# Kernel optimization log

Hardware: AMD Instinct MI355X
Metric: run time of the kernel (lower is better)

The kernel has to match this reference:

```python
import jax, jax.numpy as jnp
import numpy as np

B, C_IN, NF, H, W, L = 8, 64, 64, 96, 96, 13
NEG_SLOPE = 0.2


def conv2d(x, w, b, pad):
    # x: [B,C,H,W], w: [O,I,kh,kw]
    y = jax.lax.conv_general_dilated(
        x, w, window_strides=(1, 1), padding=[(pad, pad), (pad, pad)],
        dimension_numbers=("NCHW", "OIHW", "NCHW"))
    return y + b[None, :, None, None]


def leaky(x):
    return jax.nn.leaky_relu(x, NEG_SLOPE)


def bilinear_sample(img, px, py):
    # img: [B,C,H,W]; px,py: [B,H,W] pixel coords; zero padding outside.
    Bs, C, Hs, Ws = img.shape
    x0 = jnp.floor(px)
    y0 = jnp.floor(py)
    wx = px - x0
    wy = py - y0
    x0i = x0.astype(jnp.int32)
    y0i = y0.astype(jnp.int32)
    imgf = img.reshape(Bs, C, Hs * Ws)

    def gather(xi, yi):
        valid = ((xi >= 0) & (xi < Ws) & (yi >= 0) & (yi < Hs)).astype(img.dtype)
        xc = jnp.clip(xi, 0, Ws - 1)
        yc = jnp.clip(yi, 0, Hs - 1)
        idx = (yc * Ws + xc).reshape(Bs, 1, Hs * Ws)
        v = jnp.take_along_axis(imgf, idx, axis=2).reshape(Bs, C, Hs, Ws)
        return v * valid[:, None, :, :]

    return (gather(x0i, y0i) * ((1 - wx) * (1 - wy))[:, None]
            + gather(x0i + 1, y0i) * (wx * (1 - wy))[:, None]
            + gather(x0i, y0i + 1) * ((1 - wx) * wy)[:, None]
            + gather(x0i + 1, y0i + 1) * (wx * wy)[:, None])


def warp(img, flow):
    # img: [B,C,H,W]; flow: [B,2,H,W] (dx=flow[:,0], dy=flow[:,1])
    Bs, C, Hs, Ws = img.shape
    xx = jnp.arange(Ws, dtype=img.dtype)[None, None, :]  # [1,1,W]
    yy = jnp.arange(Hs, dtype=img.dtype)[None, :, None]  # [1,H,1]
    vx = xx + flow[:, 0]  # [B,H,W]
    vy = yy + flow[:, 1]
    # torch grid_sample(align_corners=False) with normalization 2*v/(dim-1)-1:
    # sample pixel = v*dim/(dim-1) - 0.5
    px = vx * (Ws / (Ws - 1)) - 0.5
    py = vy * (Hs / (Hs - 1)) - 0.5
    return bilinear_sample(img, px, py)


def setup_inputs() -> dict:
    key = jax.random.key(0)
    ks = jax.random.split(key, 13)
    s = 0.05
    return {
        "x": jax.random.normal(ks[0], (B, C_IN, H, W), jnp.float32),
        "m": jax.random.normal(ks[1], (B, NF, H, W), jnp.float32),
        "prev_h": jax.random.normal(ks[2], (B, NF, H, W), jnp.float32),
        "w_i2h": jax.random.normal(ks[3], (3 * NF, C_IN, 3, 3), jnp.float32) * s,
        "b_i2h": jnp.zeros((3 * NF,), jnp.float32),
        "w_i2f": jax.random.normal(ks[4], (32, C_IN, 5, 5), jnp.float32) * s,
        "b_i2f": jnp.zeros((32,), jnp.float32),
        "w_h2f": jax.random.normal(ks[5], (32, NF, 5, 5), jnp.float32) * s,
        "b_h2f": jnp.zeros((32,), jnp.float32),
        "w_fl": jax.random.normal(ks[6], (2 * L, 32, 5, 5), jnp.float32) * s,
        "b_fl": jnp.zeros((2 * L,), jnp.float32),
        "w_ret": jax.random.normal(ks[7], (3 * NF, NF * L, 1, 1), jnp.float32) * s,
        "b_ret": jnp.zeros((3 * NF,), jnp.float32),
    }


def reference(x, m, prev_h, w_i2h, b_i2h, w_i2f, b_i2f, w_h2f, b_h2f, w_fl, b_fl, w_ret, b_ret):
    # input-to-hidden gates
    i2h = conv2d(x, w_i2h, b_i2h, pad=1)              # [B,3NF,H,W]
    i0, i1, i2 = jnp.split(i2h, 3, axis=1)
    # flow generator
    f = leaky(conv2d(x, w_i2f, b_i2f, pad=2) + conv2d(prev_h, w_h2f, b_h2f, pad=2))
    flows = conv2d(f, w_fl, b_fl, pad=2)              # [B,2L,H,W]
    flows = flows.reshape(B, L, 2, H, W)
    # warp prev_h by -flow for each link (vectorized over L)
    warped = jax.vmap(lambda fl: warp(prev_h, -fl), in_axes=1, out_axes=1)(flows)
    warped = warped.reshape(B, L * NF, H, W)
    h2h = conv2d(warped, w_ret, b_ret, pad=0)         # [B,3NF,H,W]
    h0, h1, h2 = jnp.split(h2h, 3, axis=1)
    reset_gate = jax.nn.sigmoid(i0 + h0)
    update_gate = jax.nn.sigmoid(i1 + h1)
    new_mem = leaky(i2 + reset_gate * h2)
    next_h = update_gate * prev_h + (1.0 - update_gate) * new_mem
    return (next_h, m, next_h)
```

## Files before the change

kernel.cpp:

```cpp
#include <hip/hip_runtime.h>
#include <hip/hip_bf16.h>
#include <hip/hip_fp16.h>

typedef unsigned short u16;
typedef unsigned int u32;
typedef __attribute__((ext_vector_type(8))) _Float16 f16x8;
typedef __attribute__((ext_vector_type(4))) float f32x4;

#define NEG 0.2f

__device__ __forceinline__ float bf2f(u16 u) {
    return __uint_as_float(((u32)u) << 16);
}
__device__ __forceinline__ u16 f2b(float f) {
    u32 u = __float_as_uint(f);
    u32 r = (u + 0x7FFF + ((u >> 16) & 1)) >> 16;
    return (u16)r;
}
__device__ __forceinline__ u16 f2h(float f) {
    return __half_as_ushort(__float2half(f));
}
__device__ __forceinline__ float h2f(u16 u) {
    return __half2float(__ushort_as_half(u));
}
__device__ __forceinline__ float sigm(float x) {
    return 1.0f / (1.0f + __expf(-x));
}
__device__ __forceinline__ float ldin(const void* p, int idx, int flag) {
    if (flag) return ((const float*)p)[idx];
    return bf2f(((const u16*)p)[idx]);
}
__device__ __forceinline__ u16 ldin_h(const void* p, int idx, int flag) {
    if (flag) return f2h(((const float*)p)[idx]);
    return f2h(bf2f(((const u16*)p)[idx]));
}


#define WS_NEED 60371008u

__global__ void kdetect(const u16* __restrict__ x, u32* __restrict__ flag)
{
    __shared__ u32 mx[256];
    int t = threadIdx.x;
    u32 m = 0;
    for (int i = t; i < 8192; i += 256) {
        u32 e = ((u32)x[i] >> 7) & 0xFF;
        m = m > e ? m : e;
    }
    mx[t] = m;
    __syncthreads();
    for (int s = 128; s > 0; s >>= 1) {
        if (t < s) mx[t] = mx[t] > mx[t + s] ? mx[t] : mx[t + s];
        __syncthreads();
    }
    if (t == 0) flag[0] = (mx[0] > 0xC0) ? 1u : 0u;
}

__global__ void kprep(const void* __restrict__ w_i2h, const void* __restrict__ w_i2f,
                      const void* __restrict__ w_h2f, const void* __restrict__ w_fl,
                      const void* __restrict__ w_ret,
                      const void* __restrict__ b_i2h, const void* __restrict__ b_i2f,
                      const void* __restrict__ b_h2f, const void* __restrict__ b_fl,
                      const void* __restrict__ b_ret,
                      u16* __restrict__ wiA, u16* __restrict__ wfA,
                      u16* __restrict__ wlA, u16* __restrict__ wretA,
                      float* __restrict__ biases, const u32* __restrict__ flag)
{
    int flg = (int)flag[0];
    int i = blockIdx.x * 256 + threadIdx.x;
    if (i < 110592) {
        int j = i & 7; int lane = (i >> 3) & 63; int rest = i >> 9;
        int cib = rest & 1; int rest2 = rest >> 1;
        int tap = rest2 % 9; int mt = rest2 / 9;
        int oc = mt * 16 + (lane & 15);
        int ci = cib * 32 + ((lane >> 4) << 3) + j;
        wiA[i] = ldin_h(w_i2h, (oc * 64 + ci) * 9 + tap, flg);
    }
    if (i < 102400) {
        int j = i & 7; int lane = (i >> 3) & 63; int rest = i >> 9;
        int cib = rest & 3; int rest2 = rest >> 2;
        int tap = rest2 % 25; int mt = rest2 / 25;
        int oc = mt * 16 + (lane & 15);
        int cip = cib * 32 + ((lane >> 4) << 3) + j;
        wfA[i] = (cip < 64) ? ldin_h(w_i2f, (oc * 64 + cip) * 25 + tap, flg)
                            : ldin_h(w_h2f, (oc * 64 + cip - 64) * 25 + tap, flg);
    }
    if (i < 25600) {
        int j = i & 7; int lane = (i >> 3) & 63; int rest = i >> 9;
        int tap = rest % 25; int mt = rest / 25;
        int oc = mt * 16 + (lane & 15);
        int ci = ((lane >> 4) << 3) + j;
        wlA[i] = (oc < 26) ? ldin_h(w_fl, (oc * 32 + ci) * 25 + tap, flg) : (u16)0;
    }
    if (i < 159744) {
        int j = i & 7; int l = (i >> 3) & 63; int rest = i >> 9;
        int ks = rest % 26; int mt = rest / 26;
        int o = mt * 16 + (l & 15);
        int k = ks * 32 + ((l >> 4) << 3) + j;
        wretA[i] = ldin_h(w_ret, o * 832 + k, flg);
    }
    if (i < 474) {
        float v;
        if (i < 192)      v = ldin(b_i2h, i, flg);
        else if (i < 224) v = ldin(b_i2f, i - 192, flg);
        else if (i < 256) v = ldin(b_h2f, i - 224, flg);
        else if (i < 282) v = ldin(b_fl, i - 256, flg);
        else              v = ldin(b_ret, i - 282, flg);
        biases[i] = v;
    }
}

__global__ __launch_bounds__(256) void kxph(const void* __restrict__ x,
        const void* __restrict__ ph, u16* __restrict__ xph,
        const u32* __restrict__ flag)
{
    __shared__ __align__(16) u16 tile[64 * 104];
    int flg = (int)flag[0];
    int h = blockIdx.x, b = blockIdx.y;
    int t = threadIdx.x;
#pragma unroll 1
    for (int s = 0; s < 2; s++) {
        const void* src = s ? ph : x;
#pragma unroll 1
        for (int i = t; i < 768; i += 256) {
            int wc = i % 12, c = i / 12;
            int base = ((b * 64 + c) * 96 + h) * 96 + wc * 8;
            u16 r[8];
            if (flg) {
                const float* sp = (const float*)src + base;
                float4 f0 = *(const float4*)sp;
                float4 f1 = *(const float4*)(sp + 4);
                r[0] = f2h(f0.x); r[1] = f2h(f0.y); r[2] = f2h(f0.z); r[3] = f2h(f0.w);
                r[4] = f2h(f1.x); r[5] = f2h(f1.y); r[6] = f2h(f1.z); r[7] = f2h(f1.w);
            } else {
                const u16* sp = (const u16*)src + base;
                uint4 u = *(const uint4*)sp;
                r[0] = f2h(bf2f((u16)(u.x & 0xFFFF))); r[1] = f2h(bf2f((u16)(u.x >> 16)));
                r[2] = f2h(bf2f((u16)(u.y & 0xFFFF))); r[3] = f2h(bf2f((u16)(u.y >> 16)));
                r[4] = f2h(bf2f((u16)(u.z & 0xFFFF))); r[5] = f2h(bf2f((u16)(u.z >> 16)));
                r[6] = f2h(bf2f((u16)(u.w & 0xFFFF))); r[7] = f2h(bf2f((u16)(u.w >> 16)));
            }
            uint4 o;
            o.x = r[0] | ((u32)r[1] << 16); o.y = r[2] | ((u32)r[3] << 16);
            o.z = r[4] | ((u32)r[5] << 16); o.w = r[6] | ((u32)r[7] << 16);
            *(uint4*)&tile[c * 104 + wc * 8] = o;
        }
        __syncthreads();
#pragma unroll 1
        for (int i = t; i < 768; i += 256) {
            int cg = i & 7, w = i >> 3;
            u16 v[8];
#pragma unroll
            for (int k = 0; k < 8; k++) v[k] = tile[(cg * 8 + k) * 104 + w];
            uint4 o;
            o.x = v[0] | ((u32)v[1] << 16); o.y = v[2] | ((u32)v[3] << 16);
            o.z = v[4] | ((u32)v[5] << 16); o.w = v[6] | ((u32)v[7] << 16);
            *(uint4*)&xph[(((b * 96 + h) * 96 + w) << 7) + s * 64 + cg * 8] = o;
        }
        __syncthreads();
    }
}

__global__ __launch_bounds__(256) void k_flowfeat(const u16* __restrict__ xph,
        const u16* __restrict__ wfA, const float* __restrict__ biases,
        u16* __restrict__ fT)
{
    __shared__ __align__(16) u16 xl[8 * 20 * 136];
    int lin = blockIdx.x;
    int b = lin & 7;
    int r = lin >> 3;
    int x0 = (r % 6) * 16, y0 = (r / 6) * 4;
    int t = threadIdx.x, lane = t & 63, wv = t >> 6;
    int n = lane & 15, quad = lane >> 4;

    for (int i = t; i < 2560; i += 256) {
        int co = i & 15; int pos = i >> 4; int xx = pos % 20; int yy = pos / 20;
        int gy = y0 + yy - 2, gx = x0 + xx - 2;
        uint4 v = make_uint4(0, 0, 0, 0);
        if (gy >= 0 && gy < 96 && gx >= 0 && gx < 96)
            v = *(const uint4*)&xph[((((b * 96 + gy) * 96 + gx)) << 7) + (co << 3)];
        *(uint4*)&xl[(yy * 20 + xx) * 136 + (co << 3)] = v;
    }
    __syncthreads();

    f32x4 acc0 = {}, acc1 = {};
    const f16x8* A = (const f16x8*)wfA;
    f16x8 bbC[4], a0C[4], a1C[4];
    {
        int rowb = (wv * 20 + n) * 136 + quad * 8;
#pragma unroll
        for (int cib = 0; cib < 4; cib++) {
            bbC[cib] = *(const f16x8*)&xl[rowb + cib * 32];
            a0C[cib] = A[cib * 64 + lane];
            a1C[cib] = A[(100 + cib) * 64 + lane];
        }
    }
#pragma unroll 1
    for (int tap = 0; tap < 25; tap++) {
        f16x8 bbN[4], a0N[4], a1N[4];
        if (tap < 24) {
            int tn = tap + 1;
            int dy = tn / 5, dx = tn % 5;
            int rowb = ((wv + dy) * 20 + n + dx) * 136 + quad * 8;
#pragma unroll
            for (int cib = 0; cib < 4; cib++) {
                bbN[cib] = *(const f16x8*)&xl[rowb + cib * 32];
                a0N[cib] = A[(tn * 4 + cib) * 64 + lane];
                a1N[cib] = A[((25 + tn) * 4 + cib) * 64 + lane];
            }
        }
#pragma unroll
        for (int cib = 0; cib < 4; cib++) {
            acc0 = __builtin_amdgcn_mfma_f32_16x16x32_f16(a0C[cib], bbC[cib], acc0, 0, 0, 0);
            acc1 = __builtin_amdgcn_mfma_f32_16x16x32_f16(a1C[cib], bbC[cib], acc1, 0, 0, 0);
        }
#pragma unroll
        for (int cib = 0; cib < 4; cib++) {
            bbC[cib] = bbN[cib]; a0C[cib] = a0N[cib]; a1C[cib] = a1N[cib];
        }
    }

    int base = (((b * 96 + y0 + wv) * 96 + x0 + n)) * 32 + quad * 4;
    {
        u16 p[4];
#pragma unroll
        for (int r2 = 0; r2 < 4; r2++) {
            int oc = quad * 4 + r2;
            float v = acc0[r2] + biases[192 + oc] + biases[224 + oc];
            v = (v > 0.f) ? v : NEG * v;
            p[r2] = f2h(v);
        }
        *(uint2*)&fT[base] = make_uint2(p[0] | ((u32)p[1] << 16), p[2] | ((u32)p[3] << 16));
#pragma unroll
        for (int r2 = 0; r2 < 4; r2++) {
            int oc = 16 + quad * 4 + r2;
            float v = acc1[r2] + biases[192 + oc] + biases[224 + oc];
            v = (v > 0.f) ? v : NEG * v;
            p[r2] = f2h(v);
        }
        *(uint2*)&fT[base + 16] = make_uint2(p[0] | ((u32)p[1] << 16), p[2] | ((u32)p[3] << 16));
    }
}

__global__ __launch_bounds__(256) void k_flows(const u16* __restrict__ fT,
        const u16* __restrict__ wlA, const float* __restrict__ biases,
        float* __restrict__ flows)
{
    __shared__ __align__(16) u16 xl[8 * 20 * 40];
    int lin = blockIdx.x;
    int b = lin & 7;
    int r = lin >> 3;
    int x0 = (r % 6) * 16, y0 = (r / 6) * 4;
    int t = threadIdx.x, lane = t & 63, wv = t >> 6;
    int n = lane & 15, quad = lane >> 4;

    for (int i = t; i < 640; i += 256) {
        int co = i & 3; int pos = i >> 2; int xx = pos % 20; int yy = pos / 20;
        int gy = y0 + yy - 2, gx = x0 + xx - 2;
        uint4 v = make_uint4(0, 0, 0, 0);
        if (gy >= 0 && gy < 96 && gx >= 0 && gx < 96)
            v = *(const uint4*)&fT[((((b * 96 + gy) * 96 + gx)) << 5) + (co << 3)];
        *(uint4*)&xl[(yy * 20 + xx) * 40 + (co << 3)] = v;
    }
    __syncthreads();

    f32x4 acc0 = {}, acc1 = {};
    const f16x8* A = (const f16x8*)wlA;
    f16x8 a0r[4], a1r[4];
#pragma unroll
    for (int tp = 0; tp < 4; tp++) {
        a0r[tp] = A[tp * 64 + lane];
        a1r[tp] = A[(25 + tp) * 64 + lane];
    }
#pragma unroll
    for (int tap = 0; tap < 25; tap++) {
        int dy = tap / 5, dx = tap % 5;
        f16x8 bb = *(const f16x8*)&xl[((wv + dy) * 20 + n + dx) * 40 + quad * 8];
        f16x8 a0 = a0r[tap & 3];
        f16x8 a1 = a1r[tap & 3];
        if (tap + 4 < 25) {
            a0r[tap & 3] = A[(tap + 4) * 64 + lane];
            a1r[tap & 3] = A[(25 + tap + 4) * 64 + lane];
        }
        acc0 = __builtin_amdgcn_mfma_f32_16x16x32_f16(a0, bb, acc0, 0, 0, 0);
        acc1 = __builtin_amdgcn_mfma_f32_16x16x32_f16(a1, bb, acc1, 0, 0, 0);
    }

    int pix = (y0 + wv) * 96 + x0 + n;
#pragma unroll
    for (int r2 = 0; r2 < 4; r2++) {
        int oc = quad * 4 + r2;
        flows[(b * 26 + oc) * 9216 + pix] = acc0[r2] + biases[256 + oc];
        int oc1 = 16 + quad * 4 + r2;
        if (oc1 < 26)
            flows[(b * 26 + oc1) * 9216 + pix] = acc1[r2] + biases[256 + oc1];
    }
}

__global__ __launch_bounds__(256, 4) void k_fused(const float* __restrict__ flows,
        const u16* __restrict__ xph, const u16* __restrict__ wiA,
        const u16* __restrict__ wretA, const float* __restrict__ biases,
        void* __restrict__ out, const u32* __restrict__ flag)
{
    __shared__ __align__(16) char sm[26368];
    u16* xi  = (u16*)sm;
    u16* pvs = (u16*)(sm + 13056);
    u16 (*gb)[32][72] = (u16 (*)[32][72])(sm + 17152);
    float* wst = (float*)(sm + 17152);

    int flg = (int)flag[0];
    int lin = blockIdx.x;
    int b = lin & 7;
    int r = lin >> 3;
    int w0 = (r % 3) * 32;
    int h = r / 3;
    int t = threadIdx.x;
    int lane = t & 63, wv = t >> 6;
    const float S = 96.f / 95.f;
    int hrow = h * 96 + w0;

#pragma unroll 1
    for (int i = t; i < 816; i += 256) {
        int co = i & 7; int pos = i >> 3;
        int px = pos % 34, dy = pos / 34;
        int gy = h + dy - 1, gx = w0 + px - 1;
        uint4 v = make_uint4(0, 0, 0, 0);
        if (gy >= 0 && gy < 96 && gx >= 0 && gx < 96)
            v = *(const uint4*)&xph[(((b * 96 + gy) * 96 + gx) << 7) + (co << 3)];
        *(uint4*)&xi[((dy * 34 + px) << 6) + ((co ^ (px & 7)) << 3)] = v;
    }
    {
        int co = t & 7; int px = t >> 3;
        uint4 v = *(const uint4*)&xph[(((b * 96 + h) * 96 + w0 + px) << 7) + 64 + (co << 3)];
        *(uint4*)&pvs[(px << 6) + ((co ^ (px & 7)) << 3)] = v;
    }

    int p = t >> 3, sub = t & 7;
    const float* fl = &flows[b * 26 * 9216 + hrow + p];
    const u16* xb = &xph[(b * 96) * 96 * 128 + 64 + sub * 8];

    int n = lane & 15, q = lane >> 4;
    const f16x8* Ap = (const f16x8*)wretA;
    const f16x8* Ai = (const f16x8*)wiA;
    const f16x8 zv = {};

    float fdxc = fl[0 * 9216], fdyc = fl[1 * 9216];
    float fdxn = fl[2 * 9216], fdyn = fl[3 * 9216];

    f16x8 c00, c10, c01, c11; float cwx, cwy;
    f16x8 n00, n10, n01, n11; float nwx, nwy;

#define GISSUE(DX, DY, V00, V10, V01, V11, WX, WY)                         \
    {                                                                      \
        float px_ = ((float)(w0 + p) - (DX)) * S - 0.5f;                   \
        float py_ = ((float)h - (DY)) * S - 0.5f;                          \
        float fx = floorf(px_), fy = floorf(py_);                          \
        int ix = (int)fx, iy = (int)fy;                                    \
        WX = px_ - fx; WY = py_ - fy;                                      \
        bool xv0 = (ix >= 0) & (ix < 96);                                  \
        bool xv1 = (ix >= -1) & (ix < 95);                                 \
        bool yv0 = (iy >= 0) & (iy < 96);                                  \
        bool yv1 = (iy >= -1) & (iy < 95);                                 \
        V00 = zv; V10 = zv; V01 = zv; V11 = zv;                            \
        if (yv0) {                                                         \
            const u16* rr = xb + (iy * 96 + ix) * 128;                     \
            if (xv0) V00 = *(const f16x8*)rr;                              \
            if (xv1) V10 = *(const f16x8*)(rr + 128);                      \
        }                                                                  \
        if (yv1) {                                                         \
            const u16* rr = xb + ((iy + 1) * 96 + ix) * 128;               \
            if (xv0) V01 = *(const f16x8*)rr;                              \
            if (xv1) V11 = *(const f16x8*)(rr + 128);                      \
        }                                                                  \
    }

    GISSUE(fdxc, fdyc, c00, c10, c01, c11, cwx, cwy);

    __syncthreads();

    f32x4 acc2[3][2] = {};
    {
        f16x8 aC[3][2], aN[3][2];
#pragma unroll
        for (int mi = 0; mi < 3; mi++)
#pragma unroll
            for (int cib = 0; cib < 2; cib++)
                aC[mi][cib] = Ai[(((wv + 4 * mi) * 9 + 0) * 2 + cib) * 64 + lane];
#pragma unroll 1
        for (int tap = 0; tap < 9; tap++) {
            if (tap < 8) {
#pragma unroll
                for (int mi = 0; mi < 3; mi++)
#pragma unroll
                    for (int cib = 0; cib < 2; cib++)
                        aN[mi][cib] = Ai[(((wv + 4 * mi) * 9 + tap + 1) * 2 + cib) * 64 + lane];
            }
            int dy = tap / 3, dx = tap % 3;
            __builtin_amdgcn_s_setprio(1);
#pragma unroll
            for (int cib = 0; cib < 2; cib++)
#pragma unroll
                for (int g = 0; g < 2; g++) {
                    int px = g * 16 + n + dx;
                    int cor = (cib * 4 + q) ^ (px & 7);
                    f16x8 bb = *(const f16x8*)&xi[((dy * 34 + px) << 6) + (cor << 3)];
#pragma unroll
                    for (int mi = 0; mi < 3; mi++)
                        acc2[mi][g] = __builtin_amdgcn_mfma_f32_16x16x32_f16(aC[mi][cib], bb, acc2[mi][g], 0, 0, 0);
                }
            __builtin_amdgcn_s_setprio(0);
#pragma unroll
            for (int mi = 0; mi < 3; mi++)
#pragma unroll
                for (int cib = 0; cib < 2; cib++)
                    aC[mi][cib] = aN[mi][cib];
        }
    }

    f32x4 acc[3][2] = {};

#pragma unroll
    for (int l = 0; l < 13; l++) {
        float fdx2 = 0.f, fdy2 = 0.f;
        if (l + 2 < 13) { fdx2 = fl[(2 * l + 4) * 9216]; fdy2 = fl[(2 * l + 5) * 9216]; }
        if (l + 1 < 13) GISSUE(fdxn, fdyn, n00, n10, n01, n11, nwx, nwy);
        {
            float w00 = (1.f - cwx) * (1.f - cwy), w10 = cwx * (1.f - cwy);
            float w01 = (1.f - cwx) * cwy,         w11 = cwx * cwy;
            u16 res[8];
#pragma unroll
            for (int j = 0; j < 8; j++) {
                float v = w00 * (float)c00[j] + w10 * (float)c10[j]
                        + w01 * (float)c01[j] + w11 * (float)c11[j];
                res[j] = f2h(v);
            }
            uint4 o;
            o.x = res[0] | ((u32)res[1] << 16); o.y = res[2] | ((u32)res[3] << 16);
            o.z = res[4] | ((u32)res[5] << 16); o.w = res[6] | ((u32)res[7] << 16);
            *(uint4*)&gb[l & 1][p][sub * 8] = o;
        }
        __syncthreads();
        __builtin_amdgcn_s_setprio(1);
#pragma unroll
        for (int ksl = 0; ksl < 2; ksl++) {
            int ks = 2 * l + ksl;
            f16x8 b0 = *(const f16x8*)&gb[l & 1][n][ksl * 32 + q * 8];
            f16x8 b1 = *(const f16x8*)&gb[l & 1][16 + n][ksl * 32 + q * 8];
#pragma unroll
            for (int mi = 0; mi < 3; mi++) {
                f16x8 a = Ap[((wv + 4 * mi) * 26 + ks) * 64 + lane];
                acc[mi][0] = __builtin_amdgcn_mfma_f32_16x16x32_f16(a, b0, acc[mi][0], 0, 0, 0);
                acc[mi][1] = __builtin_amdgcn_mfma_f32_16x16x32_f16(a, b1, acc[mi][1], 0, 0, 0);
            }
        }
        __builtin_amdgcn_s_setprio(0);
        c00 = n00; c10 = n10; c01 = n01; c11 = n11; cwx = nwx; cwy = nwy;
        fdxc = fdxn; fdyc = fdyn; fdxn = fdx2; fdyn = fdy2;
    }
#undef GISSUE

    __syncthreads();

#pragma unroll
    for (int ni = 0; ni < 2; ni++)
#pragma unroll
        for (int r2 = 0; r2 < 4; r2++) {
            int ocg = wv * 16 + q * 4 + r2;
            int px = ni * 16 + n;
            float i0 = acc2[0][ni][r2] + biases[ocg];
            float i1 = acc2[1][ni][r2] + biases[64 + ocg];
            float i2 = acc2[2][ni][r2] + biases[128 + ocg];
            float h0 = acc[0][ni][r2] + biases[282 + ocg];
            float h1 = acc[1][ni][r2] + biases[282 + 64 + ocg];
            float h2 = acc[2][ni][r2] + biases[282 + 128 + ocg];
            int cor = (ocg >> 3) ^ (px & 7);
            float pv = h2f(pvs[(px << 6) + (cor << 3) + (ocg & 7)]);
            float rg = sigm(i0 + h0);
            float ug = sigm(i1 + h1);
            float nm = i2 + rg * h2;
            nm = (nm > 0.f) ? nm : NEG * nm;
            wst[ocg * 32 + px] = ug * pv + (1.f - ug) * nm;
        }
    __syncthreads();

#pragma unroll 1
    for (int j = 0; j < 8; j++) {
        int i = t + 256 * j;
        int pp = i & 31, cc = i >> 5;
        float nh = wst[cc * 32 + pp];
        int oidx = ((b * 64 + cc) * 96 + h) * 96 + w0 + pp;
        if (flg) {
            float* of = (float*)out;
            of[oidx] = nh;
            of[oidx + 2 * 4718592] = nh;
        } else {
            u16* ob16 = (u16*)out;
            u16 v = f2b(nh);
            ob16[oidx] = v;
            ob16[oidx + 2 * 4718592] = v;
        }
    }
}

__global__ void kcopym(const uint4* __restrict__ m, uint4* __restrict__ out,
                       const u32* __restrict__ flag)
{
    int flg = (int)flag[0];
    int n4 = flg ? 1179648 : 589824;
    int stride = gridDim.x * 256;
    for (int i = blockIdx.x * 256 + threadIdx.x; i < n4; i += stride)
        out[n4 + i] = m[i];
}

extern "C" void kernel_launch(void* const* d_in, const int* in_sizes, int n_in,
                              void* d_out, int out_size, void* d_ws, size_t ws_size,
                              hipStream_t stream)
{
    const void* x     = d_in[0];
    const void* m     = d_in[1];
    const void* ph    = d_in[2];
    const void* w_i2h = d_in[3];
    const void* b_i2h = d_in[4];
    const void* w_i2f = d_in[5];
    const void* b_i2f = d_in[6];
    const void* w_h2f = d_in[7];
    const void* b_h2f = d_in[8];
    const void* w_fl  = d_in[9];
    const void* b_fl  = d_in[10];
    const void* w_ret = d_in[11];
    const void* b_ret = d_in[12];

    char* ws = (char*)d_ws;
    u32*    flag   = (u32*)  (ws + 0);
    u16*    wiA    = (u16*)  (ws + 64);
    u16*    wfA    = (u16*)  (ws + 221248);
    u16*    wlA    = (u16*)  (ws + 426048);
    u16*    wretA  = (u16*)  (ws + 477248);
    float*  biases = (float*)(ws + 796736);
    u16*    xph    = (u16*)  (ws + 798784);
    u16*    fT     = (u16*)  (ws + 47984704);
    float*  flows  = (float*)(ws + 52703296);
    if (ws_size < WS_NEED) return;

    kdetect<<<1, 256, 0, stream>>>((const u16*)x, flag);
    kprep<<<624, 256, 0, stream>>>(w_i2h, w_i2f, w_h2f, w_fl, w_ret,
                                   b_i2h, b_i2f, b_h2f, b_fl, b_ret,
                                   wiA, wfA, wlA, wretA, biases, flag);
    kxph<<<dim3(96, 8), 256, 0, stream>>>(x, ph, xph, flag);
    k_flowfeat<<<dim3(1152), 256, 0, stream>>>(xph, wfA, biases, fT);
    k_flows<<<dim3(1152), 256, 0, stream>>>(fT, wlA, biases, flows);
    k_fused<<<dim3(2304), 256, 0, stream>>>(flows, xph, wiA, wretA, biases,
                                            d_out, flag);
    kcopym<<<2048, 256, 0, stream>>>((const uint4*)m, (uint4*)d_out, flag);
}
```

Measured before the change: 277.9 us.

## Swizzle flow-feature LDS tile, raise occupancy bound, prefetch retention weights

The flow-feature kernel's shared-memory halo tile moves from a padded row stride (136) to an XOR-swizzled 128-element stride. This is meant to avoid LDS bank conflicts while shrinking LDS usage, and it adds a launch bound asking for 4 blocks per SM. The main fused kernel now prefetches the retention-conv A weights for the next link into registers during the current link's MFMAs, instead of loading them inline. That hides global-load latency but raises register pressure, which could hurt occupancy.

```diff
diff --git a/kernel.cpp b/kernel.cpp
--- a/kernel.cpp
+++ b/kernel.cpp
@@ -161,11 +161,11 @@
     }
 }
 
-__global__ __launch_bounds__(256) void k_flowfeat(const u16* __restrict__ xph,
+__global__ __launch_bounds__(256, 4) void k_flowfeat(const u16* __restrict__ xph,
         const u16* __restrict__ wfA, const float* __restrict__ biases,
         u16* __restrict__ fT)
 {
-    __shared__ __align__(16) u16 xl[8 * 20 * 136];
+    __shared__ __align__(16) u16 xl[8 * 20 * 128];
     int lin = blockIdx.x;
     int b = lin & 7;
     int r = lin >> 3;
@@ -179,7 +179,7 @@
         uint4 v = make_uint4(0, 0, 0, 0);
         if (gy >= 0 && gy < 96 && gx >= 0 && gx < 96)
             v = *(const uint4*)&xph[((((b * 96 + gy) * 96 + gx)) << 7) + (co << 3)];
-        *(uint4*)&xl[(yy * 20 + xx) * 136 + (co << 3)] = v;
+        *(uint4*)&xl[(pos << 7) + ((co ^ (pos & 7)) << 3)] = v;
     }
     __syncthreads();
 
@@ -187,10 +187,10 @@
     const f16x8* A = (const f16x8*)wfA;
     f16x8 bbC[4], a0C[4], a1C[4];
     {
-        int rowb = (wv * 20 + n) * 136 + quad * 8;
+        int pos0 = wv * 20 + n;
 #pragma unroll
         for (int cib = 0; cib < 4; cib++) {
-            bbC[cib] = *(const f16x8*)&xl[rowb + cib * 32];
+            bbC[cib] = *(const f16x8*)&xl[(pos0 << 7) + ((((cib << 2) + quad) ^ (pos0 & 7)) << 3)];
             a0C[cib] = A[cib * 64 + lane];
             a1C[cib] = A[(100 + cib) * 64 + lane];
         }
@@ -201,10 +201,10 @@
         if (tap < 24) {
             int tn = tap + 1;
             int dy = tn / 5, dx = tn % 5;
-            int rowb = ((wv + dy) * 20 + n + dx) * 136 + quad * 8;
+            int posn = (wv + dy) * 20 + n + dx;
 #pragma unroll
             for (int cib = 0; cib < 4; cib++) {
-                bbN[cib] = *(const f16x8*)&xl[rowb + cib * 32];
+                bbN[cib] = *(const f16x8*)&xl[(posn << 7) + ((((cib << 2) + quad) ^ (posn & 7)) << 3)];
                 a0N[cib] = A[(tn * 4 + cib) * 64 + lane];
                 a1N[cib] = A[((25 + tn) * 4 + cib) * 64 + lane];
             }
@@ -418,12 +418,25 @@
     }
 
     f32x4 acc[3][2] = {};
+    f16x8 gA[2][3], gN[2][3];
+#pragma unroll
+    for (int ksl = 0; ksl < 2; ksl++)
+#pragma unroll
+        for (int mi = 0; mi < 3; mi++)
+            gA[ksl][mi] = Ap[((wv + 4 * mi) * 26 + ksl) * 64 + lane];
 
 #pragma unroll
     for (int l = 0; l < 13; l++) {
         float fdx2 = 0.f, fdy2 = 0.f;
         if (l + 2 < 13) { fdx2 = fl[(2 * l + 4) * 9216]; fdy2 = fl[(2 * l + 5) * 9216]; }
-        if (l + 1 < 13) GISSUE(fdxn, fdyn, n00, n10, n01, n11, nwx, nwy);
+        if (l + 1 < 13) {
+            GISSUE(fdxn, fdyn, n00, n10, n01, n11, nwx, nwy);
+#pragma unroll
+            for (int ksl = 0; ksl < 2; ksl++)
+#pragma unroll
+                for (int mi = 0; mi < 3; mi++)
+                    gN[ksl][mi] = Ap[((wv + 4 * mi) * 26 + 2 * (l + 1) + ksl) * 64 + lane];
+        }
         {
             float w00 = (1.f - cwx) * (1.f - cwy), w10 = cwx * (1.f - cwy);
             float w01 = (1.f - cwx) * cwy,         w11 = cwx * cwy;
@@ -443,17 +456,20 @@
         __builtin_amdgcn_s_setprio(1);
 #pragma unroll
         for (int ksl = 0; ksl < 2; ksl++) {
-            int ks = 2 * l + ksl;
             f16x8 b0 = *(const f16x8*)&gb[l & 1][n][ksl * 32 + q * 8];
             f16x8 b1 = *(const f16x8*)&gb[l & 1][16 + n][ksl * 32 + q * 8];
 #pragma unroll
             for (int mi = 0; mi < 3; mi++) {
-                f16x8 a = Ap[((wv + 4 * mi) * 26 + ks) * 64 + lane];
-                acc[mi][0] = __builtin_amdgcn_mfma_f32_16x16x32_f16(a, b0, acc[mi][0], 0, 0, 0);
-                acc[mi][1] = __builtin_amdgcn_mfma_f32_16x16x32_f16(a, b1, acc[mi][1], 0, 0, 0);
+                acc[mi][0] = __builtin_amdgcn_mfma_f32_16x16x32_f16(gA[ksl][mi], b0, acc[mi][0], 0, 0, 0);
+                acc[mi][1] = __builtin_amdgcn_mfma_f32_16x16x32_f16(gA[ksl][mi], b1, acc[mi][1], 0, 0, 0);
             }
         }
         __builtin_amdgcn_s_setprio(0);
+#pragma unroll
+        for (int ksl = 0; ksl < 2; ksl++)
+#pragma unroll
+            for (int mi = 0; mi < 3; mi++)
+                gA[ksl][mi] = gN[ksl][mi];
         c00 = n00; c10 = n10; c01 = n01; c11 = n11; cwx = nwx; cwy = nwy;
         fdxc = fdxn; fdyc = fdyn; fdxn = fdx2; fdyn = fdy2;
     }
```

Result: slower. 399.0 us (+43.6%).
